# Kernel tuning notes

Hardware: AMD Instinct MI355X
Metric: run time of the kernel (lower is better)

## Reference

```python
import jax, jax.numpy as jnp
import numpy as np

B, N, D, H = 4, 256, 32, 512

def setup_inputs() -> dict:
    key = jax.random.key(0)
    ks = jax.random.split(key, 6)
    z = jax.random.normal(ks[0], (B, N, D), dtype=jnp.float32)
    motif_mask = (jax.random.uniform(ks[1], (B, N)) > 0.5).astype(jnp.float32)
    residue_mask = jnp.ones((B, N), dtype=jnp.float32)
    # Linear weights stored as (in, out); scaled like torch default init
    W1 = jax.random.normal(ks[2], (D * D, H), dtype=jnp.float32) / np.sqrt(D * D)
    b1 = jnp.zeros((H,), dtype=jnp.float32)
    W2 = jax.random.normal(ks[3], (H, H // 2), dtype=jnp.float32) / np.sqrt(H)
    b2 = jnp.zeros((H // 2,), dtype=jnp.float32)
    W3 = jax.random.normal(ks[4], (H // 2, 1), dtype=jnp.float32) / np.sqrt(H // 2)
    b3 = jnp.zeros((1,), dtype=jnp.float32)
    return {"z": z, "motif_mask": motif_mask, "residue_mask": residue_mask,
            "W1": W1, "b1": b1, "W2": W2, "b2": b2, "W3": W3, "b3": b3}

def reference(z, motif_mask, residue_mask, W1, b1, W2, b2, W3, b3):
    # kron[b,i,j, a*D+c] = z[b,i,a] * z[b,j,c]; first Linear on kron is the
    # bilinear form z_i^T W1_h z_j -- compute via two matmuls, never
    # materializing the (B,N,N,D^2) tensor.
    d = z.shape[-1]
    W1r = W1.reshape(d, d, -1)                      # (D, D, H); axis0 = z_i dim, axis1 = z_j dim
    tmp = jnp.einsum('bia,ach->bihc', z, W1r)        # (B, N, H, D)
    h1 = jax.nn.relu(jnp.einsum('bihc,bjc->bijh', tmp, z) + b1)  # (B, N, N, H)
    h2 = jax.nn.relu(jnp.einsum('bijh,hk->bijk', h1, W2) + b2)   # (B, N, N, H/2)
    contact_logits = (jnp.einsum('bijk,ko->bijo', h2, W3) + b3)[..., 0]  # (B, N, N)
    outer_mask = motif_mask[:, None, :] * motif_mask[:, :, None]
    contact_logits = contact_logits * outer_mask
    contact_map = jax.nn.sigmoid(contact_logits)
    return (contact_map, contact_logits)
```

## Files before the change

### kernel.cpp

```cpp
#include <hip/hip_runtime.h>
#include <hip/hip_bf16.h>
#include <cstdint>
#include <cstddef>

#define NB 4
#define NN 256
#define DD 32
#define HH 512

typedef __attribute__((ext_vector_type(8))) short short8;
typedef __attribute__((ext_vector_type(4))) float f32x4;
typedef __attribute__((ext_vector_type(16))) float f32x16;

static __device__ __forceinline__ unsigned cvtpk(float a, float b) {
  unsigned r;
  asm("v_cvt_pk_bf16_f32 %0, %1, %2" : "=v"(r) : "v"(a), "v"(b));
  return r;
}
static __device__ __forceinline__ unsigned short f2bf1(float a) {
  return (unsigned short)(cvtpk(a, 0.f) & 0xffffu);
}

static __device__ __forceinline__ short8 pack8(float4 a0, float4 a1) {
  union { unsigned u[4]; short8 s; } r;
  r.u[0] = cvtpk(a0.x, a0.y); r.u[1] = cvtpk(a0.z, a0.w);
  r.u[2] = cvtpk(a1.x, a1.y); r.u[3] = cvtpk(a1.z, a1.w);
  return r.s;
}

__global__ __launch_bounds__(256) void prep0(const float* __restrict__ W1,
                                             unsigned short* __restrict__ W1F) {
  const int f = blockIdx.x * 256 + threadIdx.x;
  #pragma unroll
  for (int r = 0; r < 4; ++r) {
    int row = r * 16384 + f;
    int lane = row & 63;
    int nt = (row >> 6) & 7, w2 = (row >> 9) & 3, nblk = row >> 11;
    int quad = lane >> 4, l16 = lane & 15;
    int nl = w2 * 128 + l16 * 8 + nt;
    int hl = nl >> 5, c = nl & 31;
    const float* src = W1 + (size_t)(nblk * 16 + hl);
    float v[8];
    #pragma unroll
    for (int e = 0; e < 8; ++e)
      v[e] = src[(size_t)((quad * 8 + e) * 32 + c) * 512];
    uint4 p;
    p.x = cvtpk(v[0], v[1]); p.y = cvtpk(v[2], v[3]);
    p.z = cvtpk(v[4], v[5]); p.w = cvtpk(v[6], v[7]);
    *(uint4*)&W1F[(size_t)row * 8] = p;
  }
}

__global__ __launch_bounds__(256) void prep1(const float* __restrict__ z,
                                             const unsigned short* __restrict__ W1F,
                                             const float* __restrict__ W2,
                                             const float* __restrict__ motif,
                                             unsigned short* __restrict__ W2F,
                                             unsigned short* __restrict__ Tall,
                                             int* __restrict__ jlist,
                                             int* __restrict__ jcnt,
                                             int* __restrict__ wq,
                                             int* __restrict__ wqn,
                                             float* __restrict__ out) {
  const int blk = blockIdx.x;
  const int tid = threadIdx.x;
  if (blk < 512) {
    const int nblk = blk >> 4, mgrp = blk & 15;
    const int bibase = mgrp * 64;
    const int w2 = tid >> 6, lane = tid & 63;
    const int quad = lane >> 4, l16 = lane & 15;

    short8 bfr[8];
    #pragma unroll
    for (int nt = 0; nt < 8; ++nt)
      bfr[nt] = *(const short8*)&W1F[(size_t)((((nblk * 4 + w2) * 8) + nt) * 64 + lane) * 8];

    const int ncol = nblk * 512 + w2 * 128 + l16 * 8;
    #pragma unroll
    for (int mtg = 0; mtg < 2; ++mtg) {
      short8 afr[2];
      #pragma unroll
      for (int mi = 0; mi < 2; ++mi) {
        const float* zr = z + (size_t)(bibase + (mtg * 2 + mi) * 16 + l16) * 32 + quad * 8;
        float4 a0 = *(const float4*)(zr);
        float4 a1 = *(const float4*)(zr + 4);
        afr[mi] = pack8(a0, a1);
      }
      f32x4 d[2][8];
      #pragma unroll
      for (int mi = 0; mi < 2; ++mi)
        #pragma unroll
        for (int nt = 0; nt < 8; ++nt)
          d[mi][nt] = __builtin_amdgcn_mfma_f32_16x16x32_bf16(
              afr[mi], bfr[nt], (f32x4){0.f, 0.f, 0.f, 0.f}, 0, 0, 0);
      #pragma unroll
      for (int mi = 0; mi < 2; ++mi)
        #pragma unroll
        for (int r = 0; r < 4; ++r) {
          int rowbi = bibase + (mtg * 2 + mi) * 16 + quad * 4 + r;
          if (motif[rowbi] != 0.f) {
            uint4 p;
            p.x = cvtpk(d[mi][0][r], d[mi][1][r]);
            p.y = cvtpk(d[mi][2][r], d[mi][3][r]);
            p.z = cvtpk(d[mi][4][r], d[mi][5][r]);
            p.w = cvtpk(d[mi][6][r], d[mi][7][r]);
            *(uint4*)&Tall[(size_t)rowbi * 16384 + ncol] = p;
          }
        }
    }
  } else if (blk < 576) {
    int f8 = (blk - 512) * 256 + tid;
    int lane = f8 & 63;
    int nt = (f8 >> 6) & 1, s = (f8 >> 7) & 3, hc = (f8 >> 9) & 7, w = (f8 >> 12) & 3;
    int k2 = w * 64 + nt * 32 + (lane & 31);
    int hb = hc * 64 + s * 16 + (lane >> 5) * 8;
    float v[8];
    #pragma unroll
    for (int e = 0; e < 8; ++e) v[e] = W2[(hb + e) * 256 + k2];
    uint4 p;
    p.x = cvtpk(v[0], v[1]); p.y = cvtpk(v[2], v[3]);
    p.z = cvtpk(v[4], v[5]); p.w = cvtpk(v[6], v[7]);
    ((uint4*)W2F)[f8] = p;
  } else if (blk == 576) {
    __shared__ int itemc[4];
    __shared__ int baseh[4];
    const int w = tid >> 6, lane = tid & 63;
    int cnt = 0;
    if (w < NB) {
      #pragma unroll
      for (int ch = 0; ch < 4; ++ch) {
        int j = ch * 64 + lane;
        float m = motif[w * 256 + j];
        bool alive = (m != 0.f);
        unsigned long long mk = __ballot(alive);
        unsigned long long below = mk & ((1ull << lane) - 1ull);
        int pos = __popcll(below);
        if (alive) jlist[w * 256 + cnt + pos] = j;
        cnt += __popcll(mk);
      }
      if (lane == 0) {
        jcnt[w] = cnt;
        itemc[w] = cnt * ((cnt + 63) >> 6);
      }
    }
    __syncthreads();
    if (tid == 0) {
      int s = 0;
      #pragma unroll
      for (int k = 0; k < NB; ++k) { baseh[k] = s; s += itemc[k]; }
      *wqn = s;
    }
    __syncthreads();
    if (w < NB) {
      const int K = (cnt + 63) >> 6;
      const int base = baseh[w];
      const int L2n = cnt * K;
      int rank = 0;
      #pragma unroll
      for (int ch = 0; ch < 4; ++ch) {
        int i = ch * 64 + lane;
        bool alive = (motif[w * 256 + i] != 0.f);
        unsigned long long mk = __ballot(alive);
        unsigned long long below = mk & ((1ull << lane) - 1ull);
        int pos = __popcll(below);
        if (alive) {
          int idx0 = (rank + pos) * K;
          for (int jt = 0; jt < K; ++jt) {
            int idx = idx0 + jt;
            int nidx = idx;
            if (K == 2) {
              int g = idx >> 4;
              if (g * 16 + 16 <= L2n)
                nidx = g * 16 + ((idx & 1) << 3) + ((idx >> 1) & 7);
            }
            wq[base + nidx] = (w * 256 + i) * 4 + jt;
          }
        }
        rank += __popcll(mk);
      }
    }
  } else {
    const size_t OUT2 = (size_t)NB * NN * NN;
    const int c = blk - 577;
    for (int p = c * 4096 + tid; p < (c + 1) * 4096; p += 256) {
      int bi = p >> 8, j = p & 255, b = bi >> 8;
      if (motif[bi] == 0.f || motif[b * 256 + j] == 0.f) {
        out[p] = 0.5f;
        out[OUT2 + p] = 0.f;
      }
    }
  }
}

__global__ __launch_bounds__(256) void fused(const unsigned short* __restrict__ Tall,
                                             const unsigned short* __restrict__ W2F,
                                             const float* __restrict__ z,
                                             const float* __restrict__ b1,
                                             const float* __restrict__ b2,
                                             const float* __restrict__ W3,
                                             const float* __restrict__ b3,
                                             const float* __restrict__ motif,
                                             const int* __restrict__ jlist,
                                             const int* __restrict__ jcnt,
                                             const int* __restrict__ wq,
                                             const int* __restrict__ wqn,
                                             float* __restrict__ out) {
  __shared__ unsigned short h1s[64 * 264];
  __shared__ float red[256];

  const int bx = blockIdx.x;
  const int tid = threadIdx.x;
  const size_t OUT2 = (size_t)NB * NN * NN;
  const int nq = *wqn;

  if (bx >= nq) return;
  const int item = wq[bx];

  const int w = tid >> 6, lane = tid & 63;
  const int quad = lane >> 4, l16 = lane & 15;
  const int L = lane >> 5, c32 = lane & 31;

  const int bi = item >> 2, jt = item & 3;
  const int b = bi >> 8;
  const int cnt = jcnt[b];
  const int slotbase = jt * 64;
  const float mi_v = motif[bi];

  const unsigned short* Tbase = Tall + (size_t)bi * 16384 + (w * 16 + l16) * 32 + quad * 8;
  short8 tfr[8];
  #pragma unroll
  for (int q = 0; q < 8; ++q)
    tfr[q] = *(const short8*)(Tbase + q * 2048);

  short8 zfr[4];
  #pragma unroll
  for (int nt = 0; nt < 4; ++nt) {
    int slot = slotbase + nt * 16 + l16;
    int sc = slot < cnt ? slot : cnt - 1;
    int jj = jlist[b * 256 + sc] & 255;
    const float* zr = z + (size_t)(b * 256 + jj) * 32 + quad * 8;
    float4 a0 = *(const float4*)(zr);
    float4 a1 = *(const float4*)(zr + 4);
    zfr[nt] = pack8(a0, a1);
  }

  float b2v[2], w3v[2];
  #pragma unroll
  for (int nt = 0; nt < 2; ++nt) {
    int k2 = w * 64 + nt * 32 + c32;
    b2v[nt] = b2[k2];
    w3v[nt] = W3[k2];
  }

  f32x16 acc[2][2];
  #pragma unroll
  for (int mt = 0; mt < 2; ++mt)
    #pragma unroll
    for (int nt = 0; nt < 2; ++nt)
      acc[mt][nt] = (f32x16){0.f,0.f,0.f,0.f,0.f,0.f,0.f,0.f,
                             0.f,0.f,0.f,0.f,0.f,0.f,0.f,0.f};

  const unsigned short* Wp = W2F + w * 32768 + lane * 8;
  const float* b1base = b1 + w * 16 + quad * 4;

  #pragma unroll
  for (int half = 0; half < 2; ++half) {
    #pragma unroll
    for (int q = 0; q < 4; ++q) {
      float4 b1f = *(const float4*)(b1base + (half * 4 + q) * 64);
      f32x4 cin = {b1f.x, b1f.y, b1f.z, b1f.w};
      #pragma unroll
      for (int nt = 0; nt < 4; ++nt) {
        f32x4 d = __builtin_amdgcn_mfma_f32_16x16x32_bf16(
            tfr[half * 4 + q], zfr[nt], cin, 0, 0, 0);
        uint2 p;
        p.x = cvtpk(fmaxf(d[0], 0.f), fmaxf(d[1], 0.f));
        p.y = cvtpk(fmaxf(d[2], 0.f), fmaxf(d[3], 0.f));
        *(uint2*)&h1s[(nt * 16 + l16) * 264 + q * 64 + w * 16 + quad * 4] = p;
      }
    }
    __syncthreads();

    const unsigned short* Wh = Wp + half * 16384;
    const unsigned short* h1r = &h1s[c32 * 264 + L * 8];
    short8 bfp[4][2], afp[2][2];
    #pragma unroll
    for (int p = 0; p < 4; ++p) {
      bfp[p][0] = *(const short8*)(Wh + p * 1024);
      bfp[p][1] = *(const short8*)(Wh + p * 1024 + 512);
    }
    afp[0][0] = *(const short8*)(h1r);
    afp[0][1] = *(const short8*)(h1r + 32 * 264);
    afp[1][0] = *(const short8*)(h1r + 16);
    afp[1][1] = *(const short8*)(h1r + 32 * 264 + 16);
    #pragma unroll
    for (int u = 0; u < 16; ++u) {
      const int cur = u & 1, bq = u & 3;
      short8 a0 = afp[cur][0], a1 = afp[cur][1];
      short8 b0 = bfp[bq][0], b1q = bfp[bq][1];
      if (u < 14) {
        afp[cur][0] = *(const short8*)(h1r + (u + 2) * 16);
        afp[cur][1] = *(const short8*)(h1r + 32 * 264 + (u + 2) * 16);
      }
      if (u < 12) {
        bfp[bq][0] = *(const short8*)(Wh + (u + 4) * 1024);
        bfp[bq][1] = *(const short8*)(Wh + (u + 4) * 1024 + 512);
      }
      acc[0][0] = __builtin_amdgcn_mfma_f32_32x32x16_bf16(a0, b0, acc[0][0], 0, 0, 0);
      acc[0][1] = __builtin_amdgcn_mfma_f32_32x32x16_bf16(a0, b1q, acc[0][1], 0, 0, 0);
      acc[1][0] = __builtin_amdgcn_mfma_f32_32x32x16_bf16(a1, b0, acc[1][0], 0, 0, 0);
      acc[1][1] = __builtin_amdgcn_mfma_f32_32x32x16_bf16(a1, b1q, acc[1][1], 0, 0, 0);
    }
    if (half == 0) __syncthreads();
  }

  float pr[2][16];
  #pragma unroll
  for (int mt = 0; mt < 2; ++mt)
    #pragma unroll
    for (int reg = 0; reg < 16; ++reg) {
      float s = 0.f;
      #pragma unroll
      for (int nt = 0; nt < 2; ++nt) {
        float v = acc[mt][nt][reg] + b2v[nt];
        v = v > 0.f ? v : 0.f;
        s += v * w3v[nt];
      }
      s += __shfl_xor(s, 1);
      s += __shfl_xor(s, 2);
      s += __shfl_xor(s, 4);
      s += __shfl_xor(s, 8);
      s += __shfl_xor(s, 16);
      pr[mt][reg] = s;
    }
  if (c32 == 0) {
    #pragma unroll
    for (int mt = 0; mt < 2; ++mt)
      #pragma unroll
      for (int g = 0; g < 4; ++g) {
        float4 vv = {pr[mt][g * 4 + 0], pr[mt][g * 4 + 1],
                     pr[mt][g * 4 + 2], pr[mt][g * 4 + 3]};
        *(float4*)&red[w * 64 + mt * 32 + g * 8 + L * 4] = vv;
      }
  }
  __syncthreads();
  if (tid < 64) {
    int slot = slotbase + tid;
    if (slot < cnt) {
      int j = jlist[b * 256 + slot] & 255;
      float logit = red[tid] + red[64 + tid] + red[128 + tid] + red[192 + tid] + b3[0];
      float mm = mi_v * motif[b * 256 + j];
      logit *= mm;
      float map = 1.f / (1.f + expf(-logit));
      size_t idx = (size_t)bi * 256 + j;
      out[idx] = map;
      out[OUT2 + idx] = logit;
    }
  }
}

extern "C" void kernel_launch(void* const* d_in, const int* in_sizes, int n_in,
                              void* d_out, int out_size, void* d_ws, size_t ws_size,
                              hipStream_t stream) {
  const float* z     = (const float*)d_in[0];
  const float* motif = (const float*)d_in[1];
  const float* W1 = (const float*)d_in[3];
  const float* b1 = (const float*)d_in[4];
  const float* W2 = (const float*)d_in[5];
  const float* b2 = (const float*)d_in[6];
  const float* W3 = (const float*)d_in[7];
  const float* b3 = (const float*)d_in[8];
  float* out = (float*)d_out;

  char* ws = (char*)d_ws;
  unsigned short* Tall = (unsigned short*)ws;
  unsigned short* W2F  = (unsigned short*)(ws + 33554432);
  unsigned short* W1F  = (unsigned short*)(ws + 33554432 + 262144);
  char* tail = ws + 33554432 + 262144 + 1048576;
  int* jlist = (int*)(tail);
  int* jcnt  = (int*)(tail + 4096);
  int* wq    = (int*)(tail + 4096 + 64);
  int* wqn   = (int*)(tail + 4096 + 64 + 16384);

  prep0<<<64, 256, 0, stream>>>(W1, W1F);
  prep1<<<641, 256, 0, stream>>>(z, W1F, W2, motif, W2F, Tall,
                                 jlist, jcnt, wq, wqn, out);
  fused<<<4096, 256, 0, stream>>>(Tall, W2F, z, b1, b2, W3, b3, motif,
                                  jlist, jcnt, wq, wqn, out);
}
```

Before: 119.0 us.

## Split W2 output columns into two passes to cut registers and raise occupancy

```diff
diff --git a/kernel.cpp b/kernel.cpp
--- a/kernel.cpp
+++ b/kernel.cpp
@@ -192,7 +192,7 @@
   }
 }
 
-__global__ __launch_bounds__(256) void fused(const unsigned short* __restrict__ Tall,
+__global__ __launch_bounds__(256, 4) void fused(const unsigned short* __restrict__ Tall,
                                              const unsigned short* __restrict__ W2F,
                                              const float* __restrict__ z,
                                              const float* __restrict__ b1,
@@ -206,7 +206,7 @@
                                              const int* __restrict__ wqn,
                                              float* __restrict__ out) {
   __shared__ unsigned short h1s[64 * 264];
-  __shared__ float red[256];
+  __shared__ float red[2][256];
 
   const int bx = blockIdx.x;
   const int tid = threadIdx.x;
@@ -226,129 +226,119 @@
   const int slotbase = jt * 64;
   const float mi_v = motif[bi];
 
-  const unsigned short* Tbase = Tall + (size_t)bi * 16384 + (w * 16 + l16) * 32 + quad * 8;
-  short8 tfr[8];
-  #pragma unroll
-  for (int q = 0; q < 8; ++q)
-    tfr[q] = *(const short8*)(Tbase + q * 2048);
-
   short8 zfr[4];
   #pragma unroll
-  for (int nt = 0; nt < 4; ++nt) {
-    int slot = slotbase + nt * 16 + l16;
+  for (int sg = 0; sg < 4; ++sg) {
+    int slot = slotbase + sg * 16 + l16;
     int sc = slot < cnt ? slot : cnt - 1;
     int jj = jlist[b * 256 + sc] & 255;
     const float* zr = z + (size_t)(b * 256 + jj) * 32 + quad * 8;
     float4 a0 = *(const float4*)(zr);
     float4 a1 = *(const float4*)(zr + 4);
-    zfr[nt] = pack8(a0, a1);
-  }
-
-  float b2v[2], w3v[2];
-  #pragma unroll
-  for (int nt = 0; nt < 2; ++nt) {
-    int k2 = w * 64 + nt * 32 + c32;
-    b2v[nt] = b2[k2];
-    w3v[nt] = W3[k2];
-  }
-
-  f32x16 acc[2][2];
-  #pragma unroll
-  for (int mt = 0; mt < 2; ++mt)
-    #pragma unroll
-    for (int nt = 0; nt < 2; ++nt)
-      acc[mt][nt] = (f32x16){0.f,0.f,0.f,0.f,0.f,0.f,0.f,0.f,
-                             0.f,0.f,0.f,0.f,0.f,0.f,0.f,0.f};
-
+    zfr[sg] = pack8(a0, a1);
+  }
+
+  const unsigned short* Tbase = Tall + (size_t)bi * 16384 + (w * 16 + l16) * 32 + quad * 8;
   const unsigned short* Wp = W2F + w * 32768 + lane * 8;
   const float* b1base = b1 + w * 16 + quad * 4;
 
-  #pragma unroll
-  for (int half = 0; half < 2; ++half) {
-    #pragma unroll
-    for (int q = 0; q < 4; ++q) {
-      float4 b1f = *(const float4*)(b1base + (half * 4 + q) * 64);
-      f32x4 cin = {b1f.x, b1f.y, b1f.z, b1f.w};
-      #pragma unroll
-      for (int nt = 0; nt < 4; ++nt) {
-        f32x4 d = __builtin_amdgcn_mfma_f32_16x16x32_bf16(
-            tfr[half * 4 + q], zfr[nt], cin, 0, 0, 0);
-        uint2 p;
-        p.x = cvtpk(fmaxf(d[0], 0.f), fmaxf(d[1], 0.f));
-        p.y = cvtpk(fmaxf(d[2], 0.f), fmaxf(d[3], 0.f));
-        *(uint2*)&h1s[(nt * 16 + l16) * 264 + q * 64 + w * 16 + quad * 4] = p;
-      }
-    }
-    __syncthreads();
-
-    const unsigned short* Wh = Wp + half * 16384;
-    const unsigned short* h1r = &h1s[c32 * 264 + L * 8];
-    short8 bfp[4][2], afp[2][2];
-    #pragma unroll
-    for (int p = 0; p < 4; ++p) {
-      bfp[p][0] = *(const short8*)(Wh + p * 1024);
-      bfp[p][1] = *(const short8*)(Wh + p * 1024 + 512);
-    }
-    afp[0][0] = *(const short8*)(h1r);
-    afp[0][1] = *(const short8*)(h1r + 32 * 264);
-    afp[1][0] = *(const short8*)(h1r + 16);
-    afp[1][1] = *(const short8*)(h1r + 32 * 264 + 16);
-    #pragma unroll
-    for (int u = 0; u < 16; ++u) {
-      const int cur = u & 1, bq = u & 3;
-      short8 a0 = afp[cur][0], a1 = afp[cur][1];
-      short8 b0 = bfp[bq][0], b1q = bfp[bq][1];
-      if (u < 14) {
-        afp[cur][0] = *(const short8*)(h1r + (u + 2) * 16);
-        afp[cur][1] = *(const short8*)(h1r + 32 * 264 + (u + 2) * 16);
-      }
-      if (u < 12) {
-        bfp[bq][0] = *(const short8*)(Wh + (u + 4) * 1024);
-        bfp[bq][1] = *(const short8*)(Wh + (u + 4) * 1024 + 512);
-      }
-      acc[0][0] = __builtin_amdgcn_mfma_f32_32x32x16_bf16(a0, b0, acc[0][0], 0, 0, 0);
-      acc[0][1] = __builtin_amdgcn_mfma_f32_32x32x16_bf16(a0, b1q, acc[0][1], 0, 0, 0);
-      acc[1][0] = __builtin_amdgcn_mfma_f32_32x32x16_bf16(a1, b0, acc[1][0], 0, 0, 0);
-      acc[1][1] = __builtin_amdgcn_mfma_f32_32x32x16_bf16(a1, b1q, acc[1][1], 0, 0, 0);
-    }
-    if (half == 0) __syncthreads();
-  }
-
-  float pr[2][16];
-  #pragma unroll
-  for (int mt = 0; mt < 2; ++mt)
-    #pragma unroll
-    for (int reg = 0; reg < 16; ++reg) {
-      float s = 0.f;
-      #pragma unroll
-      for (int nt = 0; nt < 2; ++nt) {
-        float v = acc[mt][nt][reg] + b2v[nt];
-        v = v > 0.f ? v : 0.f;
-        s += v * w3v[nt];
-      }
-      s += __shfl_xor(s, 1);
-      s += __shfl_xor(s, 2);
-      s += __shfl_xor(s, 4);
-      s += __shfl_xor(s, 8);
-      s += __shfl_xor(s, 16);
-      pr[mt][reg] = s;
-    }
-  if (c32 == 0) {
-    #pragma unroll
-    for (int mt = 0; mt < 2; ++mt)
-      #pragma unroll
-      for (int g = 0; g < 4; ++g) {
-        float4 vv = {pr[mt][g * 4 + 0], pr[mt][g * 4 + 1],
-                     pr[mt][g * 4 + 2], pr[mt][g * 4 + 3]};
-        *(float4*)&red[w * 64 + mt * 32 + g * 8 + L * 4] = vv;
-      }
-  }
-  __syncthreads();
+  #pragma unroll 1
+  for (int nt = 0; nt < 2; ++nt) {
+    const int k2 = w * 64 + nt * 32 + c32;
+    const float b2s = b2[k2];
+    const float w3s = W3[k2];
+
+    f32x16 acc[2];
+    acc[0] = (f32x16){0.f,0.f,0.f,0.f,0.f,0.f,0.f,0.f,
+                      0.f,0.f,0.f,0.f,0.f,0.f,0.f,0.f};
+    acc[1] = acc[0];
+
+    #pragma unroll 1
+    for (int half = 0; half < 2; ++half) {
+      short8 tfr[4];
+      #pragma unroll
+      for (int q = 0; q < 4; ++q)
+        tfr[q] = *(const short8*)(Tbase + (half * 4 + q) * 2048);
+      #pragma unroll
+      for (int q = 0; q < 4; ++q) {
+        float4 b1f = *(const float4*)(b1base + (half * 4 + q) * 64);
+        f32x4 cin = {b1f.x, b1f.y, b1f.z, b1f.w};
+        #pragma unroll
+        for (int sg = 0; sg < 4; ++sg) {
+          f32x4 d = __builtin_amdgcn_mfma_f32_16x16x32_bf16(
+              tfr[q], zfr[sg], cin, 0, 0, 0);
+          uint2 p;
+          p.x = cvtpk(fmaxf(d[0], 0.f), fmaxf(d[1], 0.f));
+          p.y = cvtpk(fmaxf(d[2], 0.f), fmaxf(d[3], 0.f));
+          *(uint2*)&h1s[(sg * 16 + l16) * 264 + q * 64 + w * 16 + quad * 4] = p;
+        }
+      }
+      __syncthreads();
+
+      const unsigned short* Wh = Wp + half * 16384 + nt * 512;
+      const unsigned short* h1r = &h1s[c32 * 264 + L * 8];
+      short8 bfp[3], afp[2][2];
+      #pragma unroll
+      for (int p = 0; p < 3; ++p)
+        bfp[p] = *(const short8*)(Wh + p * 1024);
+      afp[0][0] = *(const short8*)(h1r);
+      afp[0][1] = *(const short8*)(h1r + 32 * 264);
+      afp[1][0] = *(const short8*)(h1r + 16);
+      afp[1][1] = *(const short8*)(h1r + 32 * 264 + 16);
+      #pragma unroll
+      for (int u = 0; u < 16; ++u) {
+        const int cur = u & 1, bq = u % 3;
+        short8 a0 = afp[cur][0], a1 = afp[cur][1];
+        short8 b0 = bfp[bq];
+        if (u < 14) {
+          afp[cur][0] = *(const short8*)(h1r + (u + 2) * 16);
+          afp[cur][1] = *(const short8*)(h1r + 32 * 264 + (u + 2) * 16);
+        }
+        if (u < 13)
+          bfp[bq] = *(const short8*)(Wh + (u + 3) * 1024);
+        acc[0] = __builtin_amdgcn_mfma_f32_32x32x16_bf16(a0, b0, acc[0], 0, 0, 0);
+        acc[1] = __builtin_amdgcn_mfma_f32_32x32x16_bf16(a1, b0, acc[1], 0, 0, 0);
+      }
+
+      if (half == 1) {
+        float pr[2][16];
+        #pragma unroll
+        for (int mt = 0; mt < 2; ++mt)
+          #pragma unroll
+          for (int reg = 0; reg < 16; ++reg) {
+            float v = acc[mt][reg] + b2s;
+            v = v > 0.f ? v : 0.f;
+            float s = v * w3s;
+            s += __shfl_xor(s, 1);
+            s += __shfl_xor(s, 2);
+            s += __shfl_xor(s, 4);
+            s += __shfl_xor(s, 8);
+            s += __shfl_xor(s, 16);
+            pr[mt][reg] = s;
+          }
+        if (c32 == 0) {
+          #pragma unroll
+          for (int mt = 0; mt < 2; ++mt)
+            #pragma unroll
+            for (int g = 0; g < 4; ++g) {
+              float4 vv = {pr[mt][g * 4 + 0], pr[mt][g * 4 + 1],
+                           pr[mt][g * 4 + 2], pr[mt][g * 4 + 3]};
+              *(float4*)&red[nt][w * 64 + mt * 32 + g * 8 + L * 4] = vv;
+            }
+        }
+      }
+      __syncthreads();
+    }
+  }
+
   if (tid < 64) {
     int slot = slotbase + tid;
     if (slot < cnt) {
       int j = jlist[b * 256 + slot] & 255;
-      float logit = red[tid] + red[64 + tid] + red[128 + tid] + red[192 + tid] + b3[0];
+      float logit = b3[0];
+      #pragma unroll
+      for (int wv = 0; wv < 4; ++wv)
+        logit += red[0][wv * 64 + tid] + red[1][wv * 64 + tid];
       float mm = mi_v * motif[b * 256 + j];
       logit *= mm;
       float map = 1.f / (1.f + expf(-logit));
```

Result: slower. 135.6 us (+13.9%).

## Double-buffer h1 in shared memory and deepen W2 register prefetch

Applied to the files above, without the earlier changes.

```diff
diff --git a/kernel.cpp b/kernel.cpp
--- a/kernel.cpp
+++ b/kernel.cpp
@@ -205,7 +205,7 @@
                                              const int* __restrict__ wq,
                                              const int* __restrict__ wqn,
                                              float* __restrict__ out) {
-  __shared__ unsigned short h1s[64 * 264];
+  __shared__ unsigned short h1s[2][64 * 264];
   __shared__ float red[256];
 
   const int bx = blockIdx.x;
@@ -227,21 +227,26 @@
   const float mi_v = motif[bi];
 
   const unsigned short* Tbase = Tall + (size_t)bi * 16384 + (w * 16 + l16) * 32 + quad * 8;
-  short8 tfr[8];
-  #pragma unroll
-  for (int q = 0; q < 8; ++q)
-    tfr[q] = *(const short8*)(Tbase + q * 2048);
+  const unsigned short* Wp = W2F + w * 32768 + lane * 8;
+  const float* b1base = b1 + w * 16 + quad * 4;
+
+  short8 bfp[8][2];
+  #pragma unroll
+  for (int p = 0; p < 8; ++p) {
+    bfp[p][0] = *(const short8*)(Wp + p * 1024);
+    bfp[p][1] = *(const short8*)(Wp + p * 1024 + 512);
+  }
 
   short8 zfr[4];
   #pragma unroll
-  for (int nt = 0; nt < 4; ++nt) {
-    int slot = slotbase + nt * 16 + l16;
+  for (int sg = 0; sg < 4; ++sg) {
+    int slot = slotbase + sg * 16 + l16;
     int sc = slot < cnt ? slot : cnt - 1;
     int jj = jlist[b * 256 + sc] & 255;
     const float* zr = z + (size_t)(b * 256 + jj) * 32 + quad * 8;
     float4 a0 = *(const float4*)(zr);
     float4 a1 = *(const float4*)(zr + 4);
-    zfr[nt] = pack8(a0, a1);
+    zfr[sg] = pack8(a0, a1);
   }
 
   float b2v[2], w3v[2];
@@ -260,58 +265,101 @@
       acc[mt][nt] = (f32x16){0.f,0.f,0.f,0.f,0.f,0.f,0.f,0.f,
                              0.f,0.f,0.f,0.f,0.f,0.f,0.f,0.f};
 
-  const unsigned short* Wp = W2F + w * 32768 + lane * 8;
-  const float* b1base = b1 + w * 16 + quad * 4;
-
-  #pragma unroll
-  for (int half = 0; half < 2; ++half) {
-    #pragma unroll
-    for (int q = 0; q < 4; ++q) {
-      float4 b1f = *(const float4*)(b1base + (half * 4 + q) * 64);
-      f32x4 cin = {b1f.x, b1f.y, b1f.z, b1f.w};
-      #pragma unroll
-      for (int nt = 0; nt < 4; ++nt) {
-        f32x4 d = __builtin_amdgcn_mfma_f32_16x16x32_bf16(
-            tfr[half * 4 + q], zfr[nt], cin, 0, 0, 0);
-        uint2 p;
-        p.x = cvtpk(fmaxf(d[0], 0.f), fmaxf(d[1], 0.f));
-        p.y = cvtpk(fmaxf(d[2], 0.f), fmaxf(d[3], 0.f));
-        *(uint2*)&h1s[(nt * 16 + l16) * 264 + q * 64 + w * 16 + quad * 4] = p;
-      }
-    }
-    __syncthreads();
-
-    const unsigned short* Wh = Wp + half * 16384;
-    const unsigned short* h1r = &h1s[c32 * 264 + L * 8];
-    short8 bfp[4][2], afp[2][2];
-    #pragma unroll
-    for (int p = 0; p < 4; ++p) {
-      bfp[p][0] = *(const short8*)(Wh + p * 1024);
-      bfp[p][1] = *(const short8*)(Wh + p * 1024 + 512);
-    }
+  short8 tfr[4];
+
+  #pragma unroll
+  for (int q = 0; q < 4; ++q)
+    tfr[q] = *(const short8*)(Tbase + q * 2048);
+  #pragma unroll
+  for (int q = 0; q < 4; ++q) {
+    float4 b1f = *(const float4*)(b1base + q * 64);
+    f32x4 cin = {b1f.x, b1f.y, b1f.z, b1f.w};
+    #pragma unroll
+    for (int sg = 0; sg < 4; ++sg) {
+      f32x4 d = __builtin_amdgcn_mfma_f32_16x16x32_bf16(tfr[q], zfr[sg], cin, 0, 0, 0);
+      uint2 p;
+      p.x = cvtpk(fmaxf(d[0], 0.f), fmaxf(d[1], 0.f));
+      p.y = cvtpk(fmaxf(d[2], 0.f), fmaxf(d[3], 0.f));
+      *(uint2*)&h1s[0][(sg * 16 + l16) * 264 + q * 64 + w * 16 + quad * 4] = p;
+    }
+  }
+  __syncthreads();
+
+  #pragma unroll
+  for (int q = 0; q < 4; ++q)
+    tfr[q] = *(const short8*)(Tbase + (4 + q) * 2048);
+  #pragma unroll
+  for (int q = 0; q < 4; ++q) {
+    float4 b1f = *(const float4*)(b1base + (4 + q) * 64);
+    f32x4 cin = {b1f.x, b1f.y, b1f.z, b1f.w};
+    #pragma unroll
+    for (int sg = 0; sg < 4; ++sg) {
+      f32x4 d = __builtin_amdgcn_mfma_f32_16x16x32_bf16(tfr[q], zfr[sg], cin, 0, 0, 0);
+      uint2 p;
+      p.x = cvtpk(fmaxf(d[0], 0.f), fmaxf(d[1], 0.f));
+      p.y = cvtpk(fmaxf(d[2], 0.f), fmaxf(d[3], 0.f));
+      *(uint2*)&h1s[1][(sg * 16 + l16) * 264 + q * 64 + w * 16 + quad * 4] = p;
+    }
+  }
+  {
+    const unsigned short* Wh = Wp;
+    const unsigned short* Wh1 = Wp + 16384;
+    const unsigned short* h1r = &h1s[0][c32 * 264 + L * 8];
+    short8 afp[2][2];
     afp[0][0] = *(const short8*)(h1r);
     afp[0][1] = *(const short8*)(h1r + 32 * 264);
     afp[1][0] = *(const short8*)(h1r + 16);
     afp[1][1] = *(const short8*)(h1r + 32 * 264 + 16);
     #pragma unroll
     for (int u = 0; u < 16; ++u) {
-      const int cur = u & 1, bq = u & 3;
+      const int cur = u & 1, bq = u & 7;
       short8 a0 = afp[cur][0], a1 = afp[cur][1];
       short8 b0 = bfp[bq][0], b1q = bfp[bq][1];
       if (u < 14) {
         afp[cur][0] = *(const short8*)(h1r + (u + 2) * 16);
         afp[cur][1] = *(const short8*)(h1r + 32 * 264 + (u + 2) * 16);
       }
-      if (u < 12) {
-        bfp[bq][0] = *(const short8*)(Wh + (u + 4) * 1024);
-        bfp[bq][1] = *(const short8*)(Wh + (u + 4) * 1024 + 512);
+      if (u < 8) {
+        bfp[bq][0] = *(const short8*)(Wh + (u + 8) * 1024);
+        bfp[bq][1] = *(const short8*)(Wh + (u + 8) * 1024 + 512);
+      } else {
+        bfp[bq][0] = *(const short8*)(Wh1 + (u - 8) * 1024);
+        bfp[bq][1] = *(const short8*)(Wh1 + (u - 8) * 1024 + 512);
       }
       acc[0][0] = __builtin_amdgcn_mfma_f32_32x32x16_bf16(a0, b0, acc[0][0], 0, 0, 0);
       acc[0][1] = __builtin_amdgcn_mfma_f32_32x32x16_bf16(a0, b1q, acc[0][1], 0, 0, 0);
       acc[1][0] = __builtin_amdgcn_mfma_f32_32x32x16_bf16(a1, b0, acc[1][0], 0, 0, 0);
       acc[1][1] = __builtin_amdgcn_mfma_f32_32x32x16_bf16(a1, b1q, acc[1][1], 0, 0, 0);
     }
-    if (half == 0) __syncthreads();
+  }
+  __syncthreads();
+
+  {
+    const unsigned short* Wh = Wp + 16384;
+    const unsigned short* h1r = &h1s[1][c32 * 264 + L * 8];
+    short8 afp[2][2];
+    afp[0][0] = *(const short8*)(h1r);
+    afp[0][1] = *(const short8*)(h1r + 32 * 264);
+    afp[1][0] = *(const short8*)(h1r + 16);
+    afp[1][1] = *(const short8*)(h1r + 32 * 264 + 16);
+    #pragma unroll
+    for (int u = 0; u < 16; ++u) {
+      const int cur = u & 1, bq = u & 7;
+      short8 a0 = afp[cur][0], a1 = afp[cur][1];
+      short8 b0 = bfp[bq][0], b1q = bfp[bq][1];
+      if (u < 14) {
+        afp[cur][0] = *(const short8*)(h1r + (u + 2) * 16);
+        afp[cur][1] = *(const short8*)(h1r + 32 * 264 + (u + 2) * 16);
+      }
+      if (u < 8) {
+        bfp[bq][0] = *(const short8*)(Wh + (u + 8) * 1024);
+        bfp[bq][1] = *(const short8*)(Wh + (u + 8) * 1024 + 512);
+      }
+      acc[0][0] = __builtin_amdgcn_mfma_f32_32x32x16_bf16(a0, b0, acc[0][0], 0, 0, 0);
+      acc[0][1] = __builtin_amdgcn_mfma_f32_32x32x16_bf16(a0, b1q, acc[0][1], 0, 0, 0);
+      acc[1][0] = __builtin_amdgcn_mfma_f32_32x32x16_bf16(a1, b0, acc[1][0], 0, 0, 0);
+      acc[1][1] = __builtin_amdgcn_mfma_f32_32x32x16_bf16(a1, b1q, acc[1][1], 0, 0, 0);
+    }
   }
 
   float pr[2][16];
```

Result: slower. 123.7 us (+4.0%).

## Double-buffer h1 in LDS and overlap first-layer MFMA with second-layer GEMM

Applied to the files above, without the earlier changes.

```diff
diff --git a/kernel.cpp b/kernel.cpp
--- a/kernel.cpp
+++ b/kernel.cpp
@@ -205,7 +205,7 @@
                                              const int* __restrict__ wq,
                                              const int* __restrict__ wqn,
                                              float* __restrict__ out) {
-  __shared__ unsigned short h1s[64 * 264];
+  __shared__ unsigned short h1s[2][64 * 136];
   __shared__ float red[256];
 
   const int bx = blockIdx.x;
@@ -227,21 +227,26 @@
   const float mi_v = motif[bi];
 
   const unsigned short* Tbase = Tall + (size_t)bi * 16384 + (w * 16 + l16) * 32 + quad * 8;
-  short8 tfr[8];
-  #pragma unroll
-  for (int q = 0; q < 8; ++q)
-    tfr[q] = *(const short8*)(Tbase + q * 2048);
+  const unsigned short* Wp = W2F + w * 32768 + lane * 8;
+  const float* b1base = b1 + w * 16 + quad * 4;
+
+  short8 bfp[8][2];
+  #pragma unroll
+  for (int p = 0; p < 8; ++p) {
+    bfp[p][0] = *(const short8*)(Wp + p * 1024);
+    bfp[p][1] = *(const short8*)(Wp + p * 1024 + 512);
+  }
 
   short8 zfr[4];
   #pragma unroll
-  for (int nt = 0; nt < 4; ++nt) {
-    int slot = slotbase + nt * 16 + l16;
+  for (int sg = 0; sg < 4; ++sg) {
+    int slot = slotbase + sg * 16 + l16;
     int sc = slot < cnt ? slot : cnt - 1;
     int jj = jlist[b * 256 + sc] & 255;
     const float* zr = z + (size_t)(b * 256 + jj) * 32 + quad * 8;
     float4 a0 = *(const float4*)(zr);
     float4 a1 = *(const float4*)(zr + 4);
-    zfr[nt] = pack8(a0, a1);
+    zfr[sg] = pack8(a0, a1);
   }
 
   float b2v[2], w3v[2];
@@ -260,90 +265,103 @@
       acc[mt][nt] = (f32x16){0.f,0.f,0.f,0.f,0.f,0.f,0.f,0.f,
                              0.f,0.f,0.f,0.f,0.f,0.f,0.f,0.f};
 
-  const unsigned short* Wp = W2F + w * 32768 + lane * 8;
-  const float* b1base = b1 + w * 16 + quad * 4;
-
-  #pragma unroll
-  for (int half = 0; half < 2; ++half) {
-    #pragma unroll
-    for (int q = 0; q < 4; ++q) {
-      float4 b1f = *(const float4*)(b1base + (half * 4 + q) * 64);
-      f32x4 cin = {b1f.x, b1f.y, b1f.z, b1f.w};
-      #pragma unroll
-      for (int nt = 0; nt < 4; ++nt) {
-        f32x4 d = __builtin_amdgcn_mfma_f32_16x16x32_bf16(
-            tfr[half * 4 + q], zfr[nt], cin, 0, 0, 0);
-        uint2 p;
-        p.x = cvtpk(fmaxf(d[0], 0.f), fmaxf(d[1], 0.f));
-        p.y = cvtpk(fmaxf(d[2], 0.f), fmaxf(d[3], 0.f));
-        *(uint2*)&h1s[(nt * 16 + l16) * 264 + q * 64 + w * 16 + quad * 4] = p;
+  #pragma unroll
+  for (int qq = 0; qq < 2; ++qq) {
+    short8 tfr = *(const short8*)(Tbase + qq * 2048);
+    float4 b1f = *(const float4*)(b1base + qq * 64);
+    f32x4 cin = {b1f.x, b1f.y, b1f.z, b1f.w};
+    #pragma unroll
+    for (int sg = 0; sg < 4; ++sg) {
+      f32x4 d = __builtin_amdgcn_mfma_f32_16x16x32_bf16(tfr, zfr[sg], cin, 0, 0, 0);
+      uint2 p;
+      p.x = cvtpk(fmaxf(d[0], 0.f), fmaxf(d[1], 0.f));
+      p.y = cvtpk(fmaxf(d[2], 0.f), fmaxf(d[3], 0.f));
+      *(uint2*)&h1s[0][(sg * 16 + l16) * 136 + qq * 64 + w * 16 + quad * 4] = p;
+    }
+  }
+  __syncthreads();
+
+  #pragma unroll
+  for (int q = 0; q < 4; ++q) {
+    if (q < 3) {
+      #pragma unroll
+      for (int qi = 0; qi < 2; ++qi) {
+        const int qq = 2 * q + 2 + qi;
+        short8 tfr = *(const short8*)(Tbase + qq * 2048);
+        float4 b1f = *(const float4*)(b1base + qq * 64);
+        f32x4 cin = {b1f.x, b1f.y, b1f.z, b1f.w};
+        #pragma unroll
+        for (int sg = 0; sg < 4; ++sg) {
+          f32x4 d = __builtin_amdgcn_mfma_f32_16x16x32_bf16(tfr, zfr[sg], cin, 0, 0, 0);
+          uint2 p;
+          p.x = cvtpk(fmaxf(d[0], 0.f), fmaxf(d[1], 0.f));
+          p.y = cvtpk(fmaxf(d[2], 0.f), fmaxf(d[3], 0.f));
+          *(uint2*)&h1s[(q + 1) & 1][(sg * 16 + l16) * 136 + qi * 64 + w * 16 + quad * 4] = p;
+        }
+      }
+    }
+    {
+      const unsigned short* h1r = &h1s[q & 1][c32 * 136 + L * 8];
+      short8 afp[2][2];
+      afp[0][0] = *(const short8*)(h1r);
+      afp[0][1] = *(const short8*)(h1r + 32 * 136);
+      afp[1][0] = *(const short8*)(h1r + 16);
+      afp[1][1] = *(const short8*)(h1r + 32 * 136 + 16);
+      #pragma unroll
+      for (int u = 0; u < 8; ++u) {
+        const int cur = u & 1;
+        short8 a0 = afp[cur][0], a1 = afp[cur][1];
+        short8 b0 = bfp[u][0], b1q = bfp[u][1];
+        if (u < 6) {
+          afp[cur][0] = *(const short8*)(h1r + (u + 2) * 16);
+          afp[cur][1] = *(const short8*)(h1r + 32 * 136 + (u + 2) * 16);
+        }
+        if (q < 3) {
+          const unsigned short* Wn = Wp + ((q + 1) >> 1) * 16384
+                                        + (8 * ((q + 1) & 1) + u) * 1024;
+          bfp[u][0] = *(const short8*)(Wn);
+          bfp[u][1] = *(const short8*)(Wn + 512);
+        }
+        acc[0][0] = __builtin_amdgcn_mfma_f32_32x32x16_bf16(a0, b0, acc[0][0], 0, 0, 0);
+        acc[0][1] = __builtin_amdgcn_mfma_f32_32x32x16_bf16(a0, b1q, acc[0][1], 0, 0, 0);
+        acc[1][0] = __builtin_amdgcn_mfma_f32_32x32x16_bf16(a1, b0, acc[1][0], 0, 0, 0);
+        acc[1][1] = __builtin_amdgcn_mfma_f32_32x32x16_bf16(a1, b1q, acc[1][1], 0, 0, 0);
+      }
+    }
+    if (q == 3) {
+      float pr[2][16];
+      #pragma unroll
+      for (int mt = 0; mt < 2; ++mt)
+        #pragma unroll
+        for (int reg = 0; reg < 16; ++reg) {
+          float s = 0.f;
+          #pragma unroll
+          for (int nt = 0; nt < 2; ++nt) {
+            float v = acc[mt][nt][reg] + b2v[nt];
+            v = v > 0.f ? v : 0.f;
+            s += v * w3v[nt];
+          }
+          s += __shfl_xor(s, 1);
+          s += __shfl_xor(s, 2);
+          s += __shfl_xor(s, 4);
+          s += __shfl_xor(s, 8);
+          s += __shfl_xor(s, 16);
+          pr[mt][reg] = s;
+        }
+      if (c32 == 0) {
+        #pragma unroll
+        for (int mt = 0; mt < 2; ++mt)
+          #pragma unroll
+          for (int g = 0; g < 4; ++g) {
+            float4 vv = {pr[mt][g * 4 + 0], pr[mt][g * 4 + 1],
+                         pr[mt][g * 4 + 2], pr[mt][g * 4 + 3]};
+            *(float4*)&red[w * 64 + mt * 32 + g * 8 + L * 4] = vv;
+          }
       }
     }
     __syncthreads();
-
-    const unsigned short* Wh = Wp + half * 16384;
-    const unsigned short* h1r = &h1s[c32 * 264 + L * 8];
-    short8 bfp[4][2], afp[2][2];
-    #pragma unroll
-    for (int p = 0; p < 4; ++p) {
-      bfp[p][0] = *(const short8*)(Wh + p * 1024);
-      bfp[p][1] = *(const short8*)(Wh + p * 1024 + 512);
-    }
-    afp[0][0] = *(const short8*)(h1r);
-    afp[0][1] = *(const short8*)(h1r + 32 * 264);
-    afp[1][0] = *(const short8*)(h1r + 16);
-    afp[1][1] = *(const short8*)(h1r + 32 * 264 + 16);
-    #pragma unroll
-    for (int u = 0; u < 16; ++u) {
-      const int cur = u & 1, bq = u & 3;
-      short8 a0 = afp[cur][0], a1 = afp[cur][1];
-      short8 b0 = bfp[bq][0], b1q = bfp[bq][1];
-      if (u < 14) {
-        afp[cur][0] = *(const short8*)(h1r + (u + 2) * 16);
-        afp[cur][1] = *(const short8*)(h1r + 32 * 264 + (u + 2) * 16);
-      }
-      if (u < 12) {
-        bfp[bq][0] = *(const short8*)(Wh + (u + 4) * 1024);
-        bfp[bq][1] = *(const short8*)(Wh + (u + 4) * 1024 + 512);
-      }
-      acc[0][0] = __builtin_amdgcn_mfma_f32_32x32x16_bf16(a0, b0, acc[0][0], 0, 0, 0);
-      acc[0][1] = __builtin_amdgcn_mfma_f32_32x32x16_bf16(a0, b1q, acc[0][1], 0, 0, 0);
-      acc[1][0] = __builtin_amdgcn_mfma_f32_32x32x16_bf16(a1, b0, acc[1][0], 0, 0, 0);
-      acc[1][1] = __builtin_amdgcn_mfma_f32_32x32x16_bf16(a1, b1q, acc[1][1], 0, 0, 0);
-    }
-    if (half == 0) __syncthreads();
-  }
-
-  float pr[2][16];
-  #pragma unroll
-  for (int mt = 0; mt < 2; ++mt)
-    #pragma unroll
-    for (int reg = 0; reg < 16; ++reg) {
-      float s = 0.f;
-      #pragma unroll
-      for (int nt = 0; nt < 2; ++nt) {
-        float v = acc[mt][nt][reg] + b2v[nt];
-        v = v > 0.f ? v : 0.f;
-        s += v * w3v[nt];
-      }
-      s += __shfl_xor(s, 1);
-      s += __shfl_xor(s, 2);
-      s += __shfl_xor(s, 4);
-      s += __shfl_xor(s, 8);
-      s += __shfl_xor(s, 16);
-      pr[mt][reg] = s;
-    }
-  if (c32 == 0) {
-    #pragma unroll
-    for (int mt = 0; mt < 2; ++mt)
-      #pragma unroll
-      for (int g = 0; g < 4; ++g) {
-        float4 vv = {pr[mt][g * 4 + 0], pr[mt][g * 4 + 1],
-                     pr[mt][g * 4 + 2], pr[mt][g * 4 + 3]};
-        *(float4*)&red[w * 64 + mt * 32 + g * 8 + L * 4] = vv;
-      }
-  }
-  __syncthreads();
+  }
+
   if (tid < 64) {
     int slot = slotbase + tid;
     if (slot < cnt) {
```

New measurement: 123.5 us. +3.8%, slower.
